# Performance work log

Measured on AMD Instinct MI355X. Metric: run time of the kernel, lower is better.

## Reference

```python
import jax, jax.numpy as jnp
import numpy as np

B, L, D = 64, 192, 1024        # batch, tokens (pre_len), in_dim
RES, DIFF, COND = 512, 256, 512
H, DH = 16, 64                 # heads, dim_head; inner = H*DH = 1024
INNER = H * DH
DFF = 4 * D                    # LinearEncoder d_ff
LC = 192                       # cond length


def setup_inputs() -> dict:
    key = jax.random.key(0)
    ks = jax.random.split(key, 16)
    n = lambda k, s, sc=1.0: jax.random.normal(k, s, dtype=jnp.float32) * sc
    return {
        "x": n(ks[0], (B, L, D)),
        "conds": n(ks[1], (B, LC, COND)),
        "diff_emb": n(ks[2], (B, DIFF)),
        "w_diff": n(ks[3], (2 * RES, DIFF), 0.02), "b_diff": jnp.zeros((2 * RES,), jnp.float32),
        "w_cond": n(ks[4], (2 * RES, COND), 0.02), "b_cond": jnp.zeros((2 * RES,), jnp.float32),
        "wq": n(ks[5], (INNER, D), 0.02),
        "wk": n(ks[6], (INNER, 2 * RES), 0.02),
        "wv": n(ks[7], (INNER, 2 * RES), 0.02),
        "wo": n(ks[8], (D, INNER), 0.02), "bo": jnp.zeros((D,), jnp.float32),
        "ln1_g": jnp.ones((D,), jnp.float32), "ln1_b": jnp.zeros((D,), jnp.float32),
        "ln2_g": jnp.ones((D,), jnp.float32), "ln2_b": jnp.zeros((D,), jnp.float32),
        "w_out": n(ks[9], (2 * D, RES), 0.02), "b_out": jnp.zeros((2 * D,), jnp.float32),
        "enc_wv": n(ks[10], (D, D), 0.02), "enc_bv": jnp.zeros((D,), jnp.float32),
        "enc_wo": n(ks[11], (D, D), 0.02), "enc_bo": jnp.zeros((D,), jnp.float32),
        "weight_mat": (jnp.eye(L, dtype=jnp.float32) + jax.random.normal(ks[12], (L, L), dtype=jnp.float32))[None],
        "conv1_w": n(ks[13], (DFF, D), 0.02), "conv1_b": jnp.zeros((DFF,), jnp.float32),
        "conv2_w": n(ks[14], (D, DFF), 0.02), "conv2_b": jnp.zeros((D,), jnp.float32),
        "enc_n1_g": jnp.ones((D,), jnp.float32), "enc_n1_b": jnp.zeros((D,), jnp.float32),
        "enc_n2_g": jnp.ones((D,), jnp.float32), "enc_n2_b": jnp.zeros((D,), jnp.float32),
    }


def _ln(x, g, b):
    m = jnp.mean(x, -1, keepdims=True)
    v = jnp.mean((x - m) ** 2, -1, keepdims=True)
    return (x - m) * jax.lax.rsqrt(v + 1e-5) * g + b


def reference(x, conds, diff_emb, w_diff, b_diff, w_cond, b_cond, wq, wk, wv, wo, bo,
              ln1_g, ln1_b, ln2_g, ln2_b, w_out, b_out, enc_wv, enc_bv, enc_wo, enc_bo,
              weight_mat, conv1_w, conv1_b, conv2_w, conv2_b,
              enc_n1_g, enc_n1_b, enc_n2_g, enc_n2_b):
    res = x
    # diff embedding broadcast-add (permute/unsqueeze in torch == add over token dim)
    x = x + (diff_emb @ w_diff.T + b_diff)[:, None, :]          # [B,L,D]
    # --- LinearEncoder (dropout is identity at inference) ---
    values = x @ enc_wv.T + enc_bv
    A = jax.nn.softplus(weight_mat[0])                          # [L,L]
    A = A / jnp.sum(A, -1, keepdims=True)                       # F.normalize(p=1)
    new_x = jnp.einsum('ij,bjd->bid', A, values)                # token mixing
    x = x + new_x @ enc_wo.T + enc_bo
    x = _ln(x, enc_n1_g, enc_n1_b)
    y = jax.nn.gelu(jnp.einsum('bld,fd->blf', x, conv1_w) + conv1_b, approximate=False)
    y = jnp.einsum('blf,df->bld', y, conv2_w) + conv2_b
    x = _ln(x + y, enc_n2_g, enc_n2_b)
    # --- norm1 + cross attention ---
    x = _ln(x, ln1_g, ln1_b)
    cond = conds @ w_cond.T + b_cond                            # [B,Lc,2*RES]
    b, l = x.shape[0], x.shape[1]
    q = (x @ wq.T).reshape(b, l, H, DH)
    k = (cond @ wk.T).reshape(b, -1, H, DH)
    v = (cond @ wv.T).reshape(b, -1, H, DH)
    scale = DH ** -0.5
    sim = jnp.einsum('bihd,bjhd->bhij', q * scale, k)           # [B,H,L,Lc]
    attn = jax.nn.softmax(sim, axis=-1)
    o = jnp.einsum('bhij,bjhd->bihd', attn, v).reshape(b, l, INNER)
    x = o @ wo.T + bo
    # --- gated residual ---
    x = _ln(x, ln2_g, ln2_b)
    gate, filt = jnp.split(x, 2, axis=2)
    x = jnp.tanh(gate) * jax.nn.sigmoid(filt)                   # [B,L,RES]
    x = x @ w_out.T + b_out                                     # [B,L,2D]
    x = jnp.where(x >= 0, x, 0.4 * x)                           # leaky_relu(0.4)
    out, skip = jnp.split(x, 2, axis=2)
    out = (res + out) / jnp.sqrt(jnp.float32(2.0))
    return out, skip
```

## Files before the change

kernel.cpp:

```cpp
#include <hip/hip_runtime.h>

typedef unsigned short ushort_t;
typedef __attribute__((ext_vector_type(8))) short bf16x8;
typedef __attribute__((ext_vector_type(4))) float f32x4;
typedef __attribute__((ext_vector_type(4))) unsigned short u16x4;

#define DEV __device__ __forceinline__

typedef const __attribute__((address_space(1))) void GV;
typedef __attribute__((address_space(3))) void SV;

DEV void gl_lds16(const ushort_t* g, ushort_t* l) {
    __builtin_amdgcn_global_load_lds((GV*)g, (SV*)l, 16, 0, 0);
}

DEV float bf2f(unsigned short u) {
    union { unsigned u; float f; } c; c.u = ((unsigned)u) << 16; return c.f;
}
DEV unsigned short f2bf(float f) {
    union { float f; unsigned u; } c; c.f = f;
    unsigned u = c.u + 0x7fffu + ((c.u >> 16) & 1u);
    return (unsigned short)(u >> 16);
}

DEV f32x4 mfma32(bf16x8 a, bf16x8 b, f32x4 c) {
    return __builtin_amdgcn_mfma_f32_16x16x32_bf16(a, b, c, 0, 0, 0);
}

#define VMCNT4  asm volatile("s_waitcnt vmcnt(4)" ::: "memory")
#define VMCNT8  asm volatile("s_waitcnt vmcnt(8)" ::: "memory")
#define VMCNT10 asm volatile("s_waitcnt vmcnt(10)" ::: "memory")
#define VMCNT0  asm volatile("s_waitcnt vmcnt(0)" ::: "memory")

struct CvtSeg { const float* src; ushort_t* dst; };
struct CvtArgs { CvtSeg s[10]; int cum[11]; };

__global__ void cvt_multi(CvtArgs a, int total4) {
    for (int i = blockIdx.x * 256 + threadIdx.x; i < total4; i += gridDim.x * 256) {
        int seg = 0;
        #pragma unroll
        for (int t = 1; t < 10; t++) if (i >= a.cum[t]) seg = t;
        int off = i - a.cum[seg];
        f32x4 v = *(const f32x4*)(a.s[seg].src + (size_t)off * 4);
        u16x4 o;
        #pragma unroll
        for (int j = 0; j < 4; j++) o[j] = f2bf(v[j]);
        *(u16x4*)(a.s[seg].dst + (size_t)off * 4) = o;
    }
}

__global__ void cvt_kernel(const float* __restrict__ in, ushort_t* __restrict__ out, int n4) {
    for (int i = blockIdx.x * 256 + threadIdx.x; i < n4; i += gridDim.x * 256) {
        f32x4 v = *(const f32x4*)(in + (size_t)i * 4);
        u16x4 o;
        #pragma unroll
        for (int j = 0; j < 4; j++) o[j] = f2bf(v[j]);
        *(u16x4*)(out + (size_t)i * 4) = o;
    }
}

__global__ void anorm_kernel(const float* __restrict__ wm, ushort_t* __restrict__ apad) {
    int row = blockIdx.x;
    int lane = threadIdx.x;
    if (row >= 192) {
        apad[row * 192 + lane] = 0;
        apad[row * 192 + lane + 64] = 0;
        apad[row * 192 + lane + 128] = 0;
        return;
    }
    float x0 = wm[row * 192 + lane];
    float x1 = wm[row * 192 + lane + 64];
    float x2 = wm[row * 192 + lane + 128];
    float s0 = (x0 > 20.f) ? x0 : log1pf(expf(x0));
    float s1 = (x1 > 20.f) ? x1 : log1pf(expf(x1));
    float s2 = (x2 > 20.f) ? x2 : log1pf(expf(x2));
    float t = s0 + s1 + s2;
    #pragma unroll
    for (int m = 1; m < 64; m <<= 1) t += __shfl_xor(t, m);
    float inv = 1.f / t;
    apad[row * 192 + lane]       = f2bf(s0 * inv);
    apad[row * 192 + lane + 64]  = f2bf(s1 * inv);
    apad[row * 192 + lane + 128] = f2bf(s2 * inv);
}

__global__ void diffproj_kernel(const float* __restrict__ emb, const float* __restrict__ w,
                                const float* __restrict__ bias, float* __restrict__ out) {
    int id = blockIdx.x * 256 + threadIdx.x;
    int b = id >> 10, n = id & 1023;
    const float* e = emb + b * 256;
    const float* wr = w + (size_t)n * 256;
    float acc = bias[n];
    for (int k2 = 0; k2 < 256; k2++) acc += e[k2] * wr[k2];
    out[id] = acc;
}

__global__ void x1_kernel(const float* __restrict__ x, const float* __restrict__ dp,
                          ushort_t* __restrict__ out) {
    const size_t N4 = 12288ULL * 1024 / 4;
    for (size_t i = (size_t)blockIdx.x * 256 + threadIdx.x; i < N4; i += (size_t)gridDim.x * 256) {
        size_t e = i * 4;
        size_t row = e >> 10;
        int d = (int)(e & 1023);
        int bb = (int)(row / 192);
        f32x4 xv = *(const f32x4*)(x + e);
        u16x4 o4;
        #pragma unroll
        for (int j = 0; j < 4; j++) o4[j] = f2bf(xv[j] + dp[bb * 1024 + d + j]);
        *(u16x4*)(out + e) = o4;
    }
}

__global__ __launch_bounds__(256) void transp_kernel(const ushort_t* __restrict__ in,
                                                     ushort_t* __restrict__ out) {
    __shared__ ushort_t t[32][33];
    int b = blockIdx.z, jt = blockIdx.y, dt = blockIdx.x;
    int tx = threadIdx.x & 31, ty = threadIdx.x >> 5;
    size_t ib = (size_t)b * 192 * 1024;
    #pragma unroll
    for (int i = 0; i < 4; i++) {
        int j = ty + i * 8;
        t[j][tx] = in[ib + (size_t)(jt * 32 + j) * 1024 + dt * 32 + tx];
    }
    __syncthreads();
    size_t ob = (size_t)b * 1024 * 192;
    #pragma unroll
    for (int i = 0; i < 4; i++) {
        int d = ty + i * 8;
        out[ob + (size_t)(dt * 32 + d) * 192 + jt * 32 + tx] = t[tx][d];
    }
}

template<int EPI>
__global__ __launch_bounds__(512, 2) void gemm256(
    const ushort_t* __restrict__ A, int lda, long long sAz,
    const ushort_t* __restrict__ W, int ldw, long long sWz,
    void* __restrict__ Cv, int ldc, long long sCz,
    int Mbound, int K,
    const float* __restrict__ bias,
    const ushort_t* __restrict__ resid,
    float scale,
    const float* __restrict__ resf)
{
    __shared__ ushort_t smem[65536];
    const int tid = threadIdx.x;
    const int wave = tid >> 6, lane = tid & 63, l15 = lane & 15, g = lane >> 4;
    const int wm = wave >> 2, wn = wave & 3;

    int bx = blockIdx.x, by = blockIdx.y;
    if (gridDim.z == 1) {
        int gx = gridDim.x, nwg = gx * gridDim.y;
        if ((nwg & 7) == 0) {
            int orig = by * gx + bx;
            int logi = (orig & 7) * (nwg >> 3) + (orig >> 3);
            bx = logi % gx; by = logi / gx;
        }
    }
    const ushort_t* Ab = A + (size_t)blockIdx.z * sAz + (size_t)by * 256 * lda;
    const ushort_t* Wb = W + (size_t)blockIdx.z * sWz + (size_t)bx * 256 * ldw;

    const int rsub  = lane >> 3;
    const int swsrc = ((lane & 7) ^ (lane >> 3)) * 8;
    const int NT = K >> 6;

    auto STAGE = [&](int kt, int buf) {
        const int k0 = kt << 6;
        ushort_t* AL = smem + buf * 16384;
        ushort_t* BL = smem + 32768 + buf * 16384;
        gl_lds16(Ab + (size_t)((wave     ) * 8 + rsub) * lda + k0 + swsrc, AL + (wave     ) * 512);
        gl_lds16(Ab + (size_t)((wave +  8) * 8 + rsub) * lda + k0 + swsrc, AL + (wave +  8) * 512);
        gl_lds16(Wb + (size_t)((wave     ) * 8 + rsub) * ldw + k0 + swsrc, BL + (wave     ) * 512);
        gl_lds16(Wb + (size_t)((wave +  8) * 8 + rsub) * ldw + k0 + swsrc, BL + (wave +  8) * 512);
        gl_lds16(Wb + (size_t)((wave + 16) * 8 + rsub) * ldw + k0 + swsrc, BL + (wave + 16) * 512);
        gl_lds16(Wb + (size_t)((wave + 24) * 8 + rsub) * ldw + k0 + swsrc, BL + (wave + 24) * 512);
        gl_lds16(Ab + (size_t)((wave + 16) * 8 + rsub) * lda + k0 + swsrc, AL + (wave + 16) * 512);
        gl_lds16(Ab + (size_t)((wave + 24) * 8 + rsub) * lda + k0 + swsrc, AL + (wave + 24) * 512);
    };

    auto LDA = [&](bf16x8 (&aa)[4][2], int mh, int buf) {
        const char* base = (const char*)smem + buf * 32768;
        #pragma unroll
        for (int m = 0; m < 4; m++) {
            int r = mh * 128 + wm * 64 + m * 16 + l15;
            #pragma unroll
            for (int kk = 0; kk < 2; kk++) {
                int byo = r * 128 + ((kk * 64 + g * 16) ^ ((l15 & 7) << 4));
                aa[m][kk] = *(const bf16x8*)(base + byo);
            }
        }
    };
    auto LDB = [&](bf16x8 (&bb)[2][2], int nh, int buf) {
        const char* base = (const char*)smem + 65536 + buf * 32768;
        #pragma unroll
        for (int n = 0; n < 2; n++) {
            int r = nh * 128 + wn * 32 + n * 16 + l15;
            #pragma unroll
            for (int kk = 0; kk < 2; kk++) {
                int byo = r * 128 + ((kk * 64 + g * 16) ^ ((l15 & 7) << 4));
                bb[n][kk] = *(const bf16x8*)(base + byo);
            }
        }
    };

    f32x4 acc[2][2][4][2] = {};
    bf16x8 afr[4][2], bfr[2][2];

    auto MM = [&](f32x4 (&aq)[4][2]) {
        __builtin_amdgcn_s_setprio(1);
        #pragma unroll
        for (int m = 0; m < 4; m++)
            #pragma unroll
            for (int n = 0; n < 2; n++)
                #pragma unroll
                for (int kk = 0; kk < 2; kk++)
                    aq[m][n] = mfma32(afr[m][kk], bfr[n][kk], aq[m][n]);
        __builtin_amdgcn_s_setprio(0);
    };

    STAGE(0, 0);
    for (int kt = 0; kt < NT; kt++) {
        const int buf = kt & 1;
        const int ktn = (kt + 1 < NT) ? kt + 1 : NT - 1;
        VMCNT4; __builtin_amdgcn_s_barrier();
        LDA(afr, 0, buf); LDB(bfr, 0, buf);
        STAGE(ktn, buf ^ 1);
        MM(acc[0][0]);
        VMCNT10; __builtin_amdgcn_s_barrier();
        LDB(bfr, 1, buf);
        MM(acc[0][1]);
        VMCNT8; __builtin_amdgcn_s_barrier();
        LDA(afr, 1, buf);
        MM(acc[1][1]);
        LDB(bfr, 0, buf);
        MM(acc[1][0]);
    }
    VMCNT0;

    #pragma unroll
    for (int mh = 0; mh < 2; mh++)
    #pragma unroll
    for (int nh = 0; nh < 2; nh++)
    #pragma unroll
    for (int m = 0; m < 4; m++)
    #pragma unroll
    for (int n = 0; n < 2; n++) {
        int Cc = bx * 256 + nh * 128 + wn * 32 + n * 16 + l15;
        float bval = 0.f;
        if (EPI == 1 || EPI == 2 || EPI == 3 || EPI == 5) bval = bias[Cc];
        #pragma unroll
        for (int q = 0; q < 4; q++) {
            int R = by * 256 + mh * 128 + wm * 64 + m * 16 + g * 4 + q;
            if (R < Mbound) {
                float t = acc[mh][nh][m][n][q];
                if (EPI == 5) {
                    t += bval;
                    t = (t >= 0.f) ? t : 0.4f * t;
                    float* Of = (float*)Cv;
                    if (Cc < 1024)
                        Of[(size_t)R * 1024 + Cc] = (resf[(size_t)R * 1024 + Cc] + t) * 0.70710678118654752f;
                    else
                        Of[12582912ULL + (size_t)R * 1024 + (Cc - 1024)] = t;
                } else {
                    ushort_t* Co = (ushort_t*)Cv + (size_t)blockIdx.z * sCz;
                    if (EPI == 1) t += bval;
                    if (EPI == 2) { t += bval; t = 0.5f * t * (1.f + erff(t * 0.70710678118654752f)); }
                    if (EPI == 3) { t += bval + bf2f(resid[(size_t)R * ldc + Cc]); }
                    if (EPI == 4) { t *= scale; }
                    Co[(size_t)R * ldc + Cc] = f2bf(t);
                }
            }
        }
    }
}

DEV void red2(float& a, float& b) {
    #pragma unroll
    for (int m = 1; m < 64; m <<= 1) { a += __shfl_xor(a, m); b += __shfl_xor(b, m); }
    __shared__ float sa[4], sb[4];
    int w = threadIdx.x >> 6;
    __syncthreads();
    if ((threadIdx.x & 63) == 0) { sa[w] = a; sb[w] = b; }
    __syncthreads();
    a = sa[0] + sa[1] + sa[2] + sa[3];
    b = sb[0] + sb[1] + sb[2] + sb[3];
}

__global__ __launch_bounds__(256) void ln_kernel(const ushort_t* __restrict__ in,
                                                 const float* __restrict__ gg, const float* __restrict__ bb,
                                                 ushort_t* __restrict__ out) {
    size_t row = blockIdx.x;
    int c0 = threadIdx.x * 4;
    u16x4 r4 = *(const u16x4*)(in + row * 1024 + c0);
    float x[4];
    float s = 0.f, sq = 0.f;
    #pragma unroll
    for (int j = 0; j < 4; j++) { x[j] = bf2f(r4[j]); s += x[j]; sq += x[j] * x[j]; }
    red2(s, sq);
    float m = s * (1.f / 1024.f);
    float var = sq * (1.f / 1024.f) - m * m;
    float rs = rsqrtf(var + 1e-5f);
    u16x4 o4;
    #pragma unroll
    for (int j = 0; j < 4; j++) o4[j] = f2bf((x[j] - m) * rs * gg[c0 + j] + bb[c0 + j]);
    *(u16x4*)(out + row * 1024 + c0) = o4;
}

__global__ __launch_bounds__(256) void ln2_kernel(const ushort_t* __restrict__ in,
                                                  const float* __restrict__ g1, const float* __restrict__ b1,
                                                  const float* __restrict__ g2, const float* __restrict__ b2,
                                                  ushort_t* __restrict__ out) {
    size_t row = blockIdx.x;
    int c0 = threadIdx.x * 4;
    u16x4 r4 = *(const u16x4*)(in + row * 1024 + c0);
    float x[4];
    float s = 0.f, sq = 0.f;
    #pragma unroll
    for (int j = 0; j < 4; j++) { x[j] = bf2f(r4[j]); s += x[j]; sq += x[j] * x[j]; }
    red2(s, sq);
    float m = s * (1.f / 1024.f);
    float var = sq * (1.f / 1024.f) - m * m;
    float rs = rsqrtf(var + 1e-5f);
    float t[4];
    float s2 = 0.f, sq2 = 0.f;
    #pragma unroll
    for (int j = 0; j < 4; j++) {
        t[j] = (x[j] - m) * rs * g1[c0 + j] + b1[c0 + j];
        s2 += t[j]; sq2 += t[j] * t[j];
    }
    red2(s2, sq2);
    float m2 = s2 * (1.f / 1024.f);
    float var2 = sq2 * (1.f / 1024.f) - m2 * m2;
    float rs2 = rsqrtf(var2 + 1e-5f);
    u16x4 o4;
    #pragma unroll
    for (int j = 0; j < 4; j++) o4[j] = f2bf((t[j] - m2) * rs2 * g2[c0 + j] + b2[c0 + j]);
    *(u16x4*)(out + row * 1024 + c0) = o4;
}

__global__ __launch_bounds__(256) void lngate_kernel(const ushort_t* __restrict__ in,
                                                     const float* __restrict__ gg, const float* __restrict__ bb,
                                                     ushort_t* __restrict__ out) {
    __shared__ float buf[1024];
    size_t row = blockIdx.x;
    int c0 = threadIdx.x * 4;
    u16x4 r4 = *(const u16x4*)(in + row * 1024 + c0);
    float x[4];
    float s = 0.f, sq = 0.f;
    #pragma unroll
    for (int j = 0; j < 4; j++) { x[j] = bf2f(r4[j]); s += x[j]; sq += x[j] * x[j]; }
    red2(s, sq);
    float m = s * (1.f / 1024.f);
    float var = sq * (1.f / 1024.f) - m * m;
    float rs = rsqrtf(var + 1e-5f);
    #pragma unroll
    for (int j = 0; j < 4; j++) buf[c0 + j] = (x[j] - m) * rs * gg[c0 + j] + bb[c0 + j];
    __syncthreads();
    if (threadIdx.x < 128) {
        int c = threadIdx.x * 4;
        u16x4 o4;
        #pragma unroll
        for (int j = 0; j < 4; j++) {
            float gv = buf[c + j], fv = buf[c + j + 512];
            o4[j] = f2bf(tanhf(gv) * (1.f / (1.f + expf(-fv))));
        }
        *(u16x4*)(out + row * 512 + c) = o4;
    }
}

__global__ __launch_bounds__(256) void attn_kernel(const ushort_t* __restrict__ q,
                                                   const ushort_t* __restrict__ k,
                                                   const ushort_t* __restrict__ v,
                                                   ushort_t* __restrict__ o, int ldkv) {
    __shared__ ushort_t vT[64][208];
    __shared__ ushort_t pS[4][16][208];
    const int tid = threadIdx.x, wave = tid >> 6, lane = tid & 63, l15 = lane & 15, g = lane >> 4;
    const int qb = blockIdx.x, h = blockIdx.y, b = blockIdx.z;
    const size_t baseq = (size_t)b * 192 * 1024 + h * 64;
    const size_t basekv = (size_t)b * 192 * ldkv + h * 64;
    #pragma unroll
    for (int it = 0; it < 6; ++it) {
        int idx = it * 256 + tid;
        int j = idx >> 3, d8 = (idx & 7) * 8;
        bf16x8 vv = *(const bf16x8*)(v + basekv + (size_t)j * ldkv + d8);
        #pragma unroll
        for (int e = 0; e < 8; e++) vT[d8 + e][j] = (ushort_t)vv[e];
    }
    const int qrow = qb * 64 + wave * 16 + l15;
    bf16x8 aq[2];
    #pragma unroll
    for (int kk = 0; kk < 2; kk++)
        aq[kk] = *(const bf16x8*)(q + baseq + (size_t)qrow * 1024 + kk * 32 + g * 8);
    f32x4 s[12] = {};
    #pragma unroll
    for (int ni = 0; ni < 12; ni++) {
        #pragma unroll
        for (int kk = 0; kk < 2; kk++) {
            bf16x8 bk = *(const bf16x8*)(k + basekv + (size_t)(ni * 16 + l15) * ldkv + kk * 32 + g * 8);
            s[ni] = mfma32(aq[kk], bk, s[ni]);
        }
    }
    float sminv[4];
    #pragma unroll
    for (int qq = 0; qq < 4; qq++) {
        float m = s[0][qq];
        #pragma unroll
        for (int ni = 1; ni < 12; ni++) m = fmaxf(m, s[ni][qq]);
        #pragma unroll
        for (int msk = 1; msk < 16; msk <<= 1) m = fmaxf(m, __shfl_xor(m, msk));
        float sum = 0.f;
        #pragma unroll
        for (int ni = 0; ni < 12; ni++) {
            float p = expf(s[ni][qq] - m);
            s[ni][qq] = p;
            sum += p;
        }
        #pragma unroll
        for (int msk = 1; msk < 16; msk <<= 1) sum += __shfl_xor(sum, msk);
        sminv[qq] = 1.f / sum;
    }
    #pragma unroll
    for (int ni = 0; ni < 12; ni++)
        #pragma unroll
        for (int qq = 0; qq < 4; qq++)
            pS[wave][g * 4 + qq][ni * 16 + l15] = f2bf(s[ni][qq]);
    __syncthreads();
    f32x4 oa[4] = {};
    #pragma unroll
    for (int ks = 0; ks < 6; ks++) {
        bf16x8 pa = *(const bf16x8*)(&pS[wave][l15][ks * 32 + g * 8]);
        #pragma unroll
        for (int di = 0; di < 4; di++) {
            bf16x8 bv = *(const bf16x8*)(&vT[di * 16 + l15][ks * 32 + g * 8]);
            oa[di] = mfma32(pa, bv, oa[di]);
        }
    }
    #pragma unroll
    for (int di = 0; di < 4; di++)
        #pragma unroll
        for (int qq = 0; qq < 4; qq++) {
            int row = qb * 64 + wave * 16 + g * 4 + qq;
            o[(size_t)b * 192 * 1024 + (size_t)row * 1024 + h * 64 + di * 16 + l15] =
                f2bf(oa[di][qq] * sminv[qq]);
        }
}

extern "C" void kernel_launch(void* const* d_in, const int* in_sizes, int n_in,
                              void* d_out, int out_size, void* d_ws, size_t ws_size,
                              hipStream_t stream) {
    (void)in_sizes; (void)n_in; (void)out_size; (void)ws_size;
    const float* x_f     = (const float*)d_in[0];
    const float* conds   = (const float*)d_in[1];
    const float* demb    = (const float*)d_in[2];
    const float* w_diff  = (const float*)d_in[3];
    const float* b_diff  = (const float*)d_in[4];
    const float* w_cond  = (const float*)d_in[5];
    const float* b_cond  = (const float*)d_in[6];
    const float* wq      = (const float*)d_in[7];
    const float* wk      = (const float*)d_in[8];
    const float* wv      = (const float*)d_in[9];
    const float* wo      = (const float*)d_in[10];
    const float* bo      = (const float*)d_in[11];
    const float* ln1_g   = (const float*)d_in[12];
    const float* ln1_b   = (const float*)d_in[13];
    const float* ln2_g   = (const float*)d_in[14];
    const float* ln2_b   = (const float*)d_in[15];
    const float* w_out   = (const float*)d_in[16];
    const float* b_out   = (const float*)d_in[17];
    const float* enc_wv  = (const float*)d_in[18];
    const float* enc_bv  = (const float*)d_in[19];
    const float* enc_wo  = (const float*)d_in[20];
    const float* enc_bo  = (const float*)d_in[21];
    const float* wmat    = (const float*)d_in[22];
    const float* conv1_w = (const float*)d_in[23];
    const float* conv1_b = (const float*)d_in[24];
    const float* conv2_w = (const float*)d_in[25];
    const float* conv2_b = (const float*)d_in[26];
    const float* en1_g   = (const float*)d_in[27];
    const float* en1_b   = (const float*)d_in[28];
    const float* en2_g   = (const float*)d_in[29];
    const float* en2_b   = (const float*)d_in[30];

    char* ws = (char*)d_ws;
    size_t off = 0;
    auto nxt = [&](size_t b) { size_t r = off; off += (b + 255) & ~(size_t)255; return r; };

    const size_t RB = 12288ULL * 1024 * 2;
    size_t o_wencv = nxt(1048576 * 2);
    size_t o_wenco = nxt(1048576 * 2);
    size_t o_conv1 = nxt(4194304 * 2);
    size_t o_conv2 = nxt(4194304 * 2);
    size_t o_wq    = nxt(1048576 * 2);
    size_t o_wkv   = nxt(2097152 * 2);
    size_t o_wo    = nxt(1048576 * 2);
    size_t o_wcond = nxt(524288 * 2);
    size_t o_wout  = nxt(1048576 * 2);
    size_t o_apad  = nxt(256 * 192 * 2);
    size_t o_dp    = nxt(64 * 1024 * 4);
    size_t o_R     = nxt(8 * RB);

    auto WS = [&](size_t o_) { return (ushort_t*)(ws + o_); };
    auto R  = [&](int i)     { return (ushort_t*)(ws + o_R + (size_t)i * RB); };

    {
        CvtArgs ca;
        const float* srcs[10] = { enc_wv, enc_wo, conv1_w, conv2_w, wq, wk, wv, wo, w_cond, w_out };
        ushort_t*    dsts[10] = { WS(o_wencv), WS(o_wenco), WS(o_conv1), WS(o_conv2), WS(o_wq),
                                  WS(o_wkv), WS(o_wkv) + 1048576, WS(o_wo), WS(o_wcond), WS(o_wout) };
        int          n4s[10]  = { 262144, 262144, 1048576, 1048576, 262144,
                                  262144, 262144, 262144, 131072, 262144 };
        int cum = 0;
        for (int i = 0; i < 10; i++) { ca.s[i].src = srcs[i]; ca.s[i].dst = dsts[i]; ca.cum[i] = cum; cum += n4s[i]; }
        ca.cum[10] = cum;
        cvt_multi<<<dim3(1024), dim3(256), 0, stream>>>(ca, cum);
    }

    anorm_kernel<<<dim3(256), dim3(64), 0, stream>>>(wmat, WS(o_apad));
    diffproj_kernel<<<dim3(256), dim3(256), 0, stream>>>(demb, w_diff, b_diff, (float*)(ws + o_dp));
    x1_kernel<<<dim3(3072), dim3(256), 0, stream>>>(x_f, (const float*)(ws + o_dp), R(0));

    gemm256<1><<<dim3(4, 48, 1), 512, 0, stream>>>(R(0), 1024, 0, WS(o_wencv), 1024, 0,
        R(1), 1024, 0, 12288, 1024, enc_bv, nullptr, 0.f, nullptr);
    transp_kernel<<<dim3(32, 6, 64), 256, 0, stream>>>(R(1), R(2));
    gemm256<0><<<dim3(4, 1, 64), 512, 0, stream>>>(WS(o_apad), 192, 0, R(2), 192, 196608LL,
        R(3), 1024, 196608LL, 192, 192, nullptr, nullptr, 0.f, nullptr);
    gemm256<3><<<dim3(4, 48, 1), 512, 0, stream>>>(R(3), 1024, 0, WS(o_wenco), 1024, 0,
        R(4), 1024, 0, 12288, 1024, enc_bo, R(0), 0.f, nullptr);
    ln_kernel<<<dim3(12288), 256, 0, stream>>>(R(4), en1_g, en1_b, R(5));
    gemm256<2><<<dim3(16, 48, 1), 512, 0, stream>>>(R(5), 1024, 0, WS(o_conv1), 1024, 0,
        R(0), 4096, 0, 12288, 1024, conv1_b, nullptr, 0.f, nullptr);
    gemm256<3><<<dim3(4, 48, 1), 512, 0, stream>>>(R(0), 4096, 0, WS(o_conv2), 4096, 0,
        R(6), 1024, 0, 12288, 4096, conv2_b, R(5), 0.f, nullptr);
    ln2_kernel<<<dim3(12288), 256, 0, stream>>>(R(6), en2_g, en2_b, ln1_g, ln1_b, R(7));
    gemm256<4><<<dim3(4, 48, 1), 512, 0, stream>>>(R(7), 1024, 0, WS(o_wq), 1024, 0,
        R(0), 1024, 0, 12288, 1024, nullptr, nullptr, 0.125f, nullptr);
    cvt_kernel<<<dim3(512), dim3(256), 0, stream>>>(conds, R(4), 6291456 / 4);
    gemm256<1><<<dim3(4, 48, 1), 512, 0, stream>>>(R(4), 512, 0, WS(o_wcond), 512, 0,
        R(5), 1024, 0, 12288, 512, b_cond, nullptr, 0.f, nullptr);
    gemm256<0><<<dim3(8, 48, 1), 512, 0, stream>>>(R(5), 1024, 0, WS(o_wkv), 1024, 0,
        R(1), 2048, 0, 12288, 1024, nullptr, nullptr, 0.f, nullptr);
    attn_kernel<<<dim3(3, 16, 64), 256, 0, stream>>>(R(0), R(1), R(1) + 1024, R(3), 2048);
    gemm256<1><<<dim3(4, 48, 1), 512, 0, stream>>>(R(3), 1024, 0, WS(o_wo), 1024, 0,
        R(6), 1024, 0, 12288, 1024, bo, nullptr, 0.f, nullptr);
    lngate_kernel<<<dim3(12288), 256, 0, stream>>>(R(6), ln2_g, ln2_b, R(4));
    gemm256<5><<<dim3(8, 48, 1), 512, 0, stream>>>(R(4), 512, 0, WS(o_wout), 512, 0,
        d_out, 1024, 0, 12288, 512, b_out, nullptr, 0.f, x_f);
}
```

Baseline: 1.151 ms.

## Restructure GEMM main loop into half-tile staged pipeline with prefetch two ahead

Splits the A and B LDS tiles into independent 128-row halves and reissues the global-to-LDS loads per half, interleaved with the four MFMA quadrants. Loads for tile t+2 go into buffer halves as soon as their fragments have been read, and B fragments are kept in separate lo/hi registers so the last quadrant reuses them without another LDS read. The goal is deeper prefetch and better overlap of memory traffic with MFMA work. In exchange it adds more barriers and explicit waitcnt/sched barriers, which costs synchronisation overhead, and the buffer-reuse ordering is easy to get wrong.

```diff
diff --git a/kernel.cpp b/kernel.cpp
--- a/kernel.cpp
+++ b/kernel.cpp
@@ -27,10 +27,11 @@
     return __builtin_amdgcn_mfma_f32_16x16x32_bf16(a, b, c, 0, 0, 0);
 }
 
-#define VMCNT4  asm volatile("s_waitcnt vmcnt(4)" ::: "memory")
-#define VMCNT8  asm volatile("s_waitcnt vmcnt(8)" ::: "memory")
-#define VMCNT10 asm volatile("s_waitcnt vmcnt(10)" ::: "memory")
+#define VMCNT6  asm volatile("s_waitcnt vmcnt(6)" ::: "memory")
 #define VMCNT0  asm volatile("s_waitcnt vmcnt(0)" ::: "memory")
+#define LGKM0   asm volatile("s_waitcnt lgkmcnt(0)" ::: "memory")
+#define SCHEDB  __builtin_amdgcn_sched_barrier(0)
+#define BAR     __builtin_amdgcn_s_barrier()
 
 struct CvtSeg { const float* src; ushort_t* dst; };
 struct CvtArgs { CvtSeg s[10]; int cum[11]; };
@@ -158,80 +159,91 @@
     const ushort_t* Ab = A + (size_t)blockIdx.z * sAz + (size_t)by * 256 * lda;
     const ushort_t* Wb = W + (size_t)blockIdx.z * sWz + (size_t)bx * 256 * ldw;
 
-    const int rsub  = lane >> 3;
-    const int swsrc = ((lane & 7) ^ (lane >> 3)) * 8;
+    const int chunkr = lane >> 3;
+    const int swsrc  = ((lane & 7) ^ chunkr) * 8;
     const int NT = K >> 6;
 
-    auto STAGE = [&](int kt, int buf) {
-        const int k0 = kt << 6;
-        ushort_t* AL = smem + buf * 16384;
-        ushort_t* BL = smem + 32768 + buf * 16384;
-        gl_lds16(Ab + (size_t)((wave     ) * 8 + rsub) * lda + k0 + swsrc, AL + (wave     ) * 512);
-        gl_lds16(Ab + (size_t)((wave +  8) * 8 + rsub) * lda + k0 + swsrc, AL + (wave +  8) * 512);
-        gl_lds16(Wb + (size_t)((wave     ) * 8 + rsub) * ldw + k0 + swsrc, BL + (wave     ) * 512);
-        gl_lds16(Wb + (size_t)((wave +  8) * 8 + rsub) * ldw + k0 + swsrc, BL + (wave +  8) * 512);
-        gl_lds16(Wb + (size_t)((wave + 16) * 8 + rsub) * ldw + k0 + swsrc, BL + (wave + 16) * 512);
-        gl_lds16(Wb + (size_t)((wave + 24) * 8 + rsub) * ldw + k0 + swsrc, BL + (wave + 24) * 512);
-        gl_lds16(Ab + (size_t)((wave + 16) * 8 + rsub) * lda + k0 + swsrc, AL + (wave + 16) * 512);
-        gl_lds16(Ab + (size_t)((wave + 24) * 8 + rsub) * lda + k0 + swsrc, AL + (wave + 24) * 512);
+    auto SH_A = [&](int tile, int half, int buf) {
+        const ushort_t* src = Ab + (size_t)(half * 128) * lda + (tile << 6) + swsrc;
+        ushort_t* dst = smem + (buf * 2 + half) * 8192;
+        int c = wave * 2;
+        gl_lds16(src + (size_t)(c * 8 + chunkr) * lda,       dst + c * 512);
+        gl_lds16(src + (size_t)((c + 1) * 8 + chunkr) * lda, dst + (c + 1) * 512);
     };
-
-    auto LDA = [&](bf16x8 (&aa)[4][2], int mh, int buf) {
-        const char* base = (const char*)smem + buf * 32768;
+    auto SH_B = [&](int tile, int half, int buf) {
+        const ushort_t* src = Wb + (size_t)(half * 128) * ldw + (tile << 6) + swsrc;
+        ushort_t* dst = smem + 32768 + (buf * 2 + half) * 8192;
+        int c = wave * 2;
+        gl_lds16(src + (size_t)(c * 8 + chunkr) * ldw,       dst + c * 512);
+        gl_lds16(src + (size_t)((c + 1) * 8 + chunkr) * ldw, dst + (c + 1) * 512);
+    };
+
+    auto LDA_ = [&](bf16x8 (&aa)[4][2], int half, int buf) {
+        const char* base = (const char*)(smem + (buf * 2 + half) * 8192);
         #pragma unroll
         for (int m = 0; m < 4; m++) {
-            int r = mh * 128 + wm * 64 + m * 16 + l15;
+            int r = wm * 64 + m * 16 + l15;
             #pragma unroll
-            for (int kk = 0; kk < 2; kk++) {
-                int byo = r * 128 + ((kk * 64 + g * 16) ^ ((l15 & 7) << 4));
-                aa[m][kk] = *(const bf16x8*)(base + byo);
-            }
+            for (int kk = 0; kk < 2; kk++)
+                aa[m][kk] = *(const bf16x8*)(base + r * 128 + ((kk * 64 + g * 16) ^ ((l15 & 7) << 4)));
         }
     };
-    auto LDB = [&](bf16x8 (&bb)[2][2], int nh, int buf) {
-        const char* base = (const char*)smem + 65536 + buf * 32768;
+    auto LDB_ = [&](bf16x8 (&bb)[2][2], int half, int buf) {
+        const char* base = (const char*)(smem + 32768 + (buf * 2 + half) * 8192);
         #pragma unroll
         for (int n = 0; n < 2; n++) {
-            int r = nh * 128 + wn * 32 + n * 16 + l15;
+            int r = wn * 32 + n * 16 + l15;
             #pragma unroll
-            for (int kk = 0; kk < 2; kk++) {
-                int byo = r * 128 + ((kk * 64 + g * 16) ^ ((l15 & 7) << 4));
-                bb[n][kk] = *(const bf16x8*)(base + byo);
-            }
+            for (int kk = 0; kk < 2; kk++)
+                bb[n][kk] = *(const bf16x8*)(base + r * 128 + ((kk * 64 + g * 16) ^ ((l15 & 7) << 4)));
         }
     };
 
     f32x4 acc[2][2][4][2] = {};
-    bf16x8 afr[4][2], bfr[2][2];
-
-    auto MM = [&](f32x4 (&aq)[4][2]) {
-        __builtin_amdgcn_s_setprio(1);
+    bf16x8 afr[4][2], blo[2][2], bhi[2][2];
+
+    auto MM = [&](f32x4 (&aq)[4][2], bf16x8 (&bb)[2][2]) {
         #pragma unroll
         for (int m = 0; m < 4; m++)
             #pragma unroll
             for (int n = 0; n < 2; n++)
                 #pragma unroll
                 for (int kk = 0; kk < 2; kk++)
-                    aq[m][n] = mfma32(afr[m][kk], bfr[n][kk], aq[m][n]);
-        __builtin_amdgcn_s_setprio(0);
+                    aq[m][n] = mfma32(afr[m][kk], bb[n][kk], aq[m][n]);
     };
 
-    STAGE(0, 0);
-    for (int kt = 0; kt < NT; kt++) {
-        const int buf = kt & 1;
-        const int ktn = (kt + 1 < NT) ? kt + 1 : NT - 1;
-        VMCNT4; __builtin_amdgcn_s_barrier();
-        LDA(afr, 0, buf); LDB(bfr, 0, buf);
-        STAGE(ktn, buf ^ 1);
-        MM(acc[0][0]);
-        VMCNT10; __builtin_amdgcn_s_barrier();
-        LDB(bfr, 1, buf);
-        MM(acc[0][1]);
-        VMCNT8; __builtin_amdgcn_s_barrier();
-        LDA(afr, 1, buf);
-        MM(acc[1][1]);
-        LDB(bfr, 0, buf);
-        MM(acc[1][0]);
+    SH_A(0, 0, 0); SH_B(0, 1, 0); SH_A(0, 1, 0); SH_B(0, 0, 0);
+    {
+        int t1 = (NT > 1) ? 1 : 0;
+        SH_A(t1, 0, 1); SH_B(t1, 1, 1); SH_A(t1, 1, 1);
+    }
+    VMCNT6;
+    BAR;
+
+    for (int t = 0; t < NT; t++) {
+        const int b = t & 1, nb = b ^ 1;
+        const int t1 = (t + 1 < NT) ? t + 1 : NT - 1;
+        const int t2 = (t + 2 < NT) ? t + 2 : NT - 1;
+        LDA_(afr, 0, b); LDB_(blo, 0, b);
+        SH_B(t1, 0, nb);
+        BAR; LGKM0; SCHEDB;
+        __builtin_amdgcn_s_setprio(1); MM(acc[0][0], blo); __builtin_amdgcn_s_setprio(0);
+        BAR;
+        LDB_(bhi, 1, b);
+        SH_A(t2, 0, b);
+        BAR; LGKM0; SCHEDB;
+        __builtin_amdgcn_s_setprio(1); MM(acc[0][1], bhi); __builtin_amdgcn_s_setprio(0);
+        BAR;
+        LDA_(afr, 1, b);
+        SH_B(t2, 1, b);
+        BAR; LGKM0; SCHEDB;
+        __builtin_amdgcn_s_setprio(1); MM(acc[1][1], bhi); __builtin_amdgcn_s_setprio(0);
+        BAR;
+        SH_A(t2, 1, b);
+        VMCNT6;
+        BAR; SCHEDB;
+        __builtin_amdgcn_s_setprio(1); MM(acc[1][0], blo); __builtin_amdgcn_s_setprio(0);
+        BAR;
     }
     VMCNT0;
 
```

New measurement: 1.129 ms. About the same (-1.9%).
